# Performance work log

Hardware: AMD Instinct MI355X
Metric: run time of the kernel (lower is better)

Reference implementation:

```python
import jax, jax.numpy as jnp
import numpy as np

B, S, D = 2, 11253, 256
NHEAD, NLEVEL, DFF = 8, 4, 1024
KERNEL = 2
NPOINT = KERNEL * KERNEL
HEAD_DIM = D // NHEAD
LEVEL_SHAPES = [(92, 92), (46, 46), (23, 23), (12, 12)]
LEVEL_STARTS = np.cumsum([0] + [h * w for h, w in LEVEL_SHAPES])[:-1]


def _kernel_indices():
    # BoxeR _create_kernel_indices: even kernel -> [-0.5, 0.5]/K, (x, y) order
    idx = np.arange(KERNEL, dtype=np.float32) - (KERNEL - 1) / 2.0
    i, j = np.meshgrid(idx, idx, indexing="ij")
    return jnp.asarray(np.stack([j, i], -1).reshape(-1, 2) / KERNEL)


KIDX = _kernel_indices()  # (NPOINT, 2) box-relative sample offsets


def layer_norm(x, w, b, eps=1e-5):
    mu = x.mean(-1, keepdims=True)
    var = ((x - mu) ** 2).mean(-1, keepdims=True)
    return (x - mu) * jax.lax.rsqrt(var + eps) * w + b


def setup_inputs() -> dict:
    key = jax.random.key(0)
    ks = jax.random.split(key, 12)

    def p(i, shape, scale=0.02):
        return jax.random.normal(ks[i], shape, jnp.float32) * scale

    cxcy = jax.random.uniform(ks[2], (B, S, 2), jnp.float32, minval=0.1, maxval=0.9)
    wh = jax.random.uniform(ks[3], (B, S, 2), jnp.float32, minval=0.02, maxval=0.2)
    return dict(
        src=jax.random.normal(ks[0], (B, S, D), jnp.float32),
        pos=jax.random.normal(ks[1], (B, S, D), jnp.float32),
        src_shape=jnp.asarray(np.array(LEVEL_SHAPES, np.int32)),
        src_mask=jnp.zeros((B, S), jnp.bool_),
        src_start_index=jnp.asarray(LEVEL_STARTS.astype(np.int32)),
        src_valid_ratios=jnp.ones((B, NLEVEL, 2), jnp.float32),
        ref_windows=jnp.concatenate([cxcy, wh], -1),
        value_w=p(4, (D, D)), value_b=jnp.zeros((D,), jnp.float32),
        out_w=p(5, (D, D)), out_b=jnp.zeros((D,), jnp.float32),
        box_w=p(6, (NHEAD * NLEVEL * 4, D)), box_b=jnp.zeros((NHEAD * NLEVEL * 4,), jnp.float32),
        attn_w=p(7, (NHEAD * NLEVEL * NPOINT, D)), attn_b=jnp.zeros((NHEAD * NLEVEL * NPOINT,), jnp.float32),
        lin1_w=p(8, (DFF, D)), lin1_b=jnp.zeros((DFF,), jnp.float32),
        lin2_w=p(9, (D, DFF)), lin2_b=jnp.zeros((D,), jnp.float32),
        norm1_w=jnp.ones((D,), jnp.float32), norm1_b=jnp.zeros((D,), jnp.float32),
        norm2_w=jnp.ones((D,), jnp.float32), norm2_b=jnp.zeros((D,), jnp.float32),
    )


def box_attention(q, src, src_mask, src_valid_ratios, ref_windows,
                  value_w, value_b, out_w, out_b, box_w, box_b, attn_w, attn_b):
    value = src @ value_w.T + value_b
    value = jnp.where(src_mask[..., None], 0.0, value)
    value = value.reshape(B, S, NHEAD, HEAD_DIM)

    # where-to-attend: per-head, per-level box offsets decoded around ref_windows (cx,cy,w,h)
    off = (q @ box_w.T + box_b).reshape(B, S, NHEAD, NLEVEL, 4)
    ref = ref_windows[:, :, None, None, :]
    boxes = ref + off / 8.0 * ref[..., jnp.array([2, 3, 2, 3])]
    center, size = boxes[..., None, :2], boxes[..., None, 2:]
    grid = center + KIDX * jax.nn.relu(size)  # (B,S,nh,L,P,2) in normalized [0,1] coords
    grid = grid * src_valid_ratios[:, None, None, :, None, :]

    attn = (q @ attn_w.T + attn_b).reshape(B, S, NHEAD, NLEVEL * NPOINT)
    attn = jax.nn.softmax(attn, -1).reshape(B, S, NHEAD, NLEVEL, NPOINT)

    out = jnp.zeros((B, NHEAD, S, HEAD_DIM), src.dtype)
    for lvl, (H, W) in enumerate(LEVEL_SHAPES):
        s0 = int(LEVEL_STARTS[lvl])
        v = jnp.transpose(value[:, s0:s0 + H * W], (0, 2, 1, 3))  # (B,nh,HW,hd)
        loc = jnp.transpose(grid[:, :, :, lvl], (0, 2, 1, 3, 4))  # (B,nh,S,P,2)
        # grid_sample bilinear, align_corners=False, zero padding
        px = loc[..., 0] * W - 0.5
        py = loc[..., 1] * H - 0.5
        x0, y0 = jnp.floor(px), jnp.floor(py)
        wx, wy = (px - x0)[..., None], (py - y0)[..., None]

        def gather(ix, iy):
            valid = (ix >= 0) & (ix < W) & (iy >= 0) & (iy < H)
            idx = (jnp.clip(iy, 0, H - 1) * W + jnp.clip(ix, 0, W - 1)).astype(jnp.int32)
            g = jnp.take_along_axis(v, idx.reshape(B, NHEAD, S * NPOINT)[..., None], axis=2)
            return g.reshape(B, NHEAD, S, NPOINT, HEAD_DIM) * valid[..., None]

        g00, g01 = gather(x0, y0), gather(x0 + 1, y0)
        g10, g11 = gather(x0, y0 + 1), gather(x0 + 1, y0 + 1)
        samp = (g00 * (1 - wx) + g01 * wx) * (1 - wy) + (g10 * (1 - wx) + g11 * wx) * wy
        aw = jnp.transpose(attn[:, :, :, lvl], (0, 2, 1, 3))  # (B,nh,S,P)
        out = out + jnp.einsum("bhspd,bhsp->bhsd", samp, aw)

    out = jnp.transpose(out, (0, 2, 1, 3)).reshape(B, S, D)
    return out @ out_w.T + out_b


def reference(src, pos, src_shape, src_mask, src_start_index, src_valid_ratios,
              ref_windows, value_w, value_b, out_w, out_b, box_w, box_b,
              attn_w, attn_b, lin1_w, lin1_b, lin2_w, lin2_b,
              norm1_w, norm1_b, norm2_w, norm2_b):
    # self-attn (box attention) + residual + LN
    src2 = box_attention(src + pos, src, src_mask, src_valid_ratios, ref_windows,
                         value_w, value_b, out_w, out_b, box_w, box_b, attn_w, attn_b)
    x = layer_norm(src + src2, norm1_w, norm1_b)
    # FFN + residual + LN (dropout=0 in eval)
    ff = jax.nn.relu(x @ lin1_w.T + lin1_b) @ lin2_w.T + lin2_b
    return layer_norm(x + ff, norm2_w, norm2_b)
```

## Files before the change

### kernel.cpp

```cpp
#include <hip/hip_runtime.h>
#include <hip/hip_bf16.h>
#include <hip/hip_fp16.h>

#define TOKENS 22506
#define SLEN   11253

typedef __bf16 bf16x8 __attribute__((ext_vector_type(8)));
typedef float  f32x4  __attribute__((ext_vector_type(4)));
typedef float  f32x2  __attribute__((ext_vector_type(2)));
typedef uint   u32x4  __attribute__((ext_vector_type(4)));

#if defined(__has_builtin)
#if __has_builtin(__builtin_amdgcn_cvt_pk_f32_fp8) && __has_builtin(__builtin_amdgcn_cvt_pk_fp8_f32)
#define HAS_FP8CVT 1
#endif
#endif

__device__ __forceinline__ ushort f2bu(float f) {
    __hip_bfloat16 h = __float2bfloat16(f);
    return *reinterpret_cast<ushort*>(&h);
}
__device__ __forceinline__ float bu2f(ushort u) {
    return __uint_as_float((uint)u << 16);
}
__device__ __forceinline__ uint pkf16(float a, float b) {
    __half2 h = __floats2half2_rn(a, b);
    return *reinterpret_cast<uint*>(&h);
}
__device__ __forceinline__ void gl16(const ushort* g, ushort* l) {
    __builtin_amdgcn_global_load_lds(
        (__attribute__((address_space(1))) void*)(g),
        (__attribute__((address_space(3))) void*)(l), 16, 0, 0);
}

#ifndef HAS_FP8CVT
__device__ __forceinline__ uint enc_fp8(float x) {
    if (!(fabsf(x) >= 0.f)) return 0;
    uint u = __float_as_uint(x);
    uint s = (u >> 24) & 0x80u;
    float ax = fabsf(x);
    if (ax >= 448.f) return s | 0x7Eu;
    if (ax < 0.0009765625f) return s;
    int e; frexpf(ax, &e);
    int ue = e - 1;
    if (ue < -6) {
        int m = (int)(ax * 512.f + 0.5f);
        if (m > 7) m = 7;
        return s | (uint)m;
    }
    float q = ax * exp2f((float)(3 - ue));
    int mi = (int)(q + 0.5f);
    if (mi >= 16) { mi >>= 1; ++ue; if (ue > 8) return s | 0x7Eu; }
    return s | ((uint)(ue + 7) << 3) | ((uint)mi & 7u);
}
__device__ __forceinline__ float dec_fp8(uint b) {
    const float sgn = (b & 0x80u) ? -1.f : 1.f;
    const uint e = (b >> 3) & 15u, m = b & 7u;
    if (e == 0) return sgn * (float)m * 0.001953125f;
    return sgn * (1.0f + (float)m * 0.125f) * exp2f((float)e - 7.f);
}
#endif

__device__ __forceinline__ uint fp8pack4(float f0, float f1, float f2, float f3) {
#ifdef HAS_FP8CVT
    int p = 0;
    p = __builtin_amdgcn_cvt_pk_fp8_f32(f0, f1, p, false);
    p = __builtin_amdgcn_cvt_pk_fp8_f32(f2, f3, p, true);
    return (uint)p;
#else
    return enc_fp8(f0) | (enc_fp8(f1) << 8) | (enc_fp8(f2) << 16) | (enc_fp8(f3) << 24);
#endif
}
template<bool HI>
__device__ __forceinline__ f32x2 fp8pair(uint w) {
#ifdef HAS_FP8CVT
    auto c = __builtin_amdgcn_cvt_pk_f32_fp8((int)w, HI);
    f32x2 r; r.x = c[0]; r.y = c[1]; return r;
#else
    const uint sh = HI ? 16u : 0u;
    f32x2 r; r.x = dec_fp8((w >> sh) & 0xFFu); r.y = dec_fp8((w >> (sh + 8)) & 0xFFu);
    return r;
#endif
}

template<bool RELU, bool NTSTORE, bool F8Z0>
__global__ __launch_bounds__(256) void gemm_small(
    const ushort* __restrict__ A0, const ushort* __restrict__ W0,
    const float* __restrict__ b0, void* __restrict__ C0,
    const ushort* __restrict__ A1, const ushort* __restrict__ W1,
    const float* __restrict__ b1, void* __restrict__ C1,
    int M, int N, int K)
{
    const bool zz = blockIdx.z != 0;
    const ushort* A   = zz ? A1 : A0;
    const ushort* W   = zz ? W1 : W0;
    const float* bias = zz ? b1 : b0;
    void* Cptr        = zz ? C1 : C0;

    __shared__ ushort smem[12288];
    const int tid  = threadIdx.x;
    const int lane = tid & 63;
    const int wid  = tid >> 6;
    const int wr = wid >> 1, wc = wid & 1;
    const int m0 = blockIdx.x * 64, n0 = blockIdx.y * 128;
    const int lrow = lane & 15, lhi = lane >> 4;

    const int arow = tid >> 2;
    const int scol = (tid & 3) << 3;
    const ushort* ga  = A + (size_t)min(m0 + arow, M - 1) * K + scol;
    const ushort* gb0 = W + (size_t)(n0 + arow)      * K + scol;
    const ushort* gb1 = W + (size_t)(n0 + arow + 64) * K + scol;

    f32x4 acc[2][4] = {};
    const int NT = K >> 5;

    gl16(ga,  &smem[tid * 8]);
    gl16(gb0, &smem[4096 + tid * 8]);
    gl16(gb1, &smem[4096 + tid * 8 + 2048]);

    int cur = 0;
    for (int t = 0; t < NT; ++t) {
        __syncthreads();
        if (t + 1 < NT) {
            const int k0 = (t + 1) << 5;
            const int nb = cur ^ 1;
            gl16(ga  + k0, &smem[nb * 2048 + tid * 8]);
            gl16(gb0 + k0, &smem[4096 + nb * 4096 + tid * 8]);
            gl16(gb1 + k0, &smem[4096 + nb * 4096 + tid * 8 + 2048]);
        }
        bf16x8 afr[2], bfr[4];
        #pragma unroll
        for (int m = 0; m < 2; ++m)
            afr[m] = *reinterpret_cast<const bf16x8*>(
                &smem[cur * 2048 + (wr * 32 + m * 16 + lrow) * 32 + lhi * 8]);
        #pragma unroll
        for (int n = 0; n < 4; ++n)
            bfr[n] = *reinterpret_cast<const bf16x8*>(
                &smem[4096 + cur * 4096 + (wc * 64 + n * 16 + lrow) * 32 + lhi * 8]);
        #pragma unroll
        for (int m = 0; m < 2; ++m)
            #pragma unroll
            for (int n = 0; n < 4; ++n)
                acc[m][n] = __builtin_amdgcn_mfma_f32_16x16x32_bf16(
                    afr[m], bfr[n], acc[m][n], 0, 0, 0);
        cur ^= 1;
    }

    __syncthreads();
    #pragma unroll
    for (int m = 0; m < 2; ++m) {
        #pragma unroll
        for (int n = 0; n < 4; ++n) {
            const int col = wc * 64 + n * 16 + lrow;
            const float bv = bias[n0 + col];
            #pragma unroll
            for (int r = 0; r < 4; ++r) {
                const int row = wr * 32 + m * 16 + lhi * 4 + r;
                float v = acc[m][n][r] + bv;
                if (RELU) v = fmaxf(v, 0.f);
                smem[row * 136 + col] = f2bu(v);
            }
        }
    }
    __syncthreads();
    if (F8Z0 && !zz) {
        #pragma unroll
        for (int i = 0; i < 4; ++i) {
            const int e = tid + i * 256;
            const int row = e >> 4, ch = e & 15;
            if (m0 + row < M) {
                const u32x4 v = *reinterpret_cast<const u32x4*>(&smem[row * 136 + ch * 8]);
                float f[8];
                #pragma unroll
                for (int j = 0; j < 4; ++j) {
                    f[2 * j]     = __uint_as_float(v[j] << 16);
                    f[2 * j + 1] = __uint_as_float(v[j] & 0xFFFF0000u);
                }
                uint2 o;
                o.x = fp8pack4(f[0], f[1], f[2], f[3]);
                o.y = fp8pack4(f[4], f[5], f[6], f[7]);
                *reinterpret_cast<uint2*>(
                    (unsigned char*)Cptr + (size_t)(m0 + row) * N + n0 + ch * 8) = o;
            }
        }
    } else {
        #pragma unroll
        for (int i = 0; i < 4; ++i) {
            const int e = tid + i * 256;
            const int row = e >> 4, ch = e & 15;
            if (m0 + row < M) {
                const u32x4 v = *reinterpret_cast<const u32x4*>(&smem[row * 136 + ch * 8]);
                u32x4* dst = reinterpret_cast<u32x4*>(
                    (ushort*)Cptr + (size_t)(m0 + row) * N + n0 + ch * 8);
                if (NTSTORE) __builtin_nontemporal_store(v, dst);
                else *dst = v;
            }
        }
    }
}

__global__ __launch_bounds__(256) void prep_all(
    const float* __restrict__ vw, const float* __restrict__ bw,
    const float* __restrict__ aw, const float* __restrict__ ow,
    const float* __restrict__ l1, const float* __restrict__ l2,
    const float* __restrict__ bb, const float* __restrict__ ab,
    ushort* __restrict__ dstW, float* __restrict__ dstQB,
    const float4* __restrict__ src, const float4* __restrict__ pos,
    ushort4* __restrict__ srcb, ushort4* __restrict__ qb)
{
    const int blk = blockIdx.x;
    if (blk < 2817) {
        const int i = blk * 256 + threadIdx.x;
        if (i < 720896) {
            float v;
            if      (i <  65536) v = vw[i];
            else if (i <  98304) v = bw[i -  65536];
            else if (i < 131072) v = aw[i -  98304];
            else if (i < 196608) v = ow[i - 131072];
            else if (i < 458752) v = l1[i - 196608];
            else                 v = l2[i - 458752];
            dstW[i] = f2bu(v);
        } else if (i < 721152) {
            const int j = i - 720896;
            dstQB[j] = (j < 128) ? bb[j] : ab[j - 128];
        }
    } else {
        const int i = (blk - 2817) * 256 + threadIdx.x;
        if (i >= TOKENS * 64) return;
        const float4 s = src[i], p = pos[i];
        ushort4 us, uq;
        us.x = f2bu(s.x); us.y = f2bu(s.y); us.z = f2bu(s.z); us.w = f2bu(s.w);
        uq.x = f2bu(s.x + p.x); uq.y = f2bu(s.y + p.y);
        uq.z = f2bu(s.z + p.z); uq.w = f2bu(s.w + p.w);
        srcb[i] = us; qb[i] = uq;
    }
}

__global__ __launch_bounds__(256) void box_fused(
    const unsigned char* __restrict__ val,
    const ushort* __restrict__ qout,
    const float* __restrict__ refw,
    const float* __restrict__ vratio,
    ushort* __restrict__ attnout)
{
    __shared__ ushort4 offs[64 * 17];
    __shared__ uint2 wts[64 * 17];
    const int tid = threadIdx.x;

    int work;
    {
        const int x = blockIdx.x & 7, s = blockIdx.x >> 3;
        work = (x < 4) ? (s * 4 + x) : (1408 + s * 4 + (x - 4));
        if ((int)gridDim.x != 2814 || work >= (int)gridDim.x) work = blockIdx.x;
    }
    const int t0 = work * 8;

    {
        const int u = tid >> 2, lvl = tid & 3;
        const int t = min(t0 + (u >> 3), TOKENS - 1);
        const int h = u & 7;
        const int b = (t >= SLEN) ? 1 : 0;
        const ushort* qr = qout + (size_t)t * 256;

        const uint2 lu = *reinterpret_cast<const uint2*>(qr + 128 + h * 16 + lvl * 4);
        float e0 = __uint_as_float(lu.x << 16);
        float e1 = __uint_as_float(lu.x & 0xFFFF0000u);
        float e2 = __uint_as_float(lu.y << 16);
        float e3 = __uint_as_float(lu.y & 0xFFFF0000u);
        float mx = fmaxf(fmaxf(e0, e1), fmaxf(e2, e3));
        mx = fmaxf(mx, __shfl_xor(mx, 1));
        mx = fmaxf(mx, __shfl_xor(mx, 2));
        e0 = __expf(e0 - mx); e1 = __expf(e1 - mx);
        e2 = __expf(e2 - mx); e3 = __expf(e3 - mx);
        float ss = e0 + e1 + e2 + e3;
        ss += __shfl_xor(ss, 1);
        ss += __shfl_xor(ss, 2);
        const float inv = 1.f / ss;
        const float pe[4] = { e0 * inv, e1 * inv, e2 * inv, e3 * inv };

        const uint2 ou = *reinterpret_cast<const uint2*>(qr + h * 16 + lvl * 4);
        const float o0 = __uint_as_float(ou.x << 16) * 0.125f;
        const float o1 = __uint_as_float(ou.x & 0xFFFF0000u) * 0.125f;
        const float o2 = __uint_as_float(ou.y << 16) * 0.125f;
        const float o3 = __uint_as_float(ou.y & 0xFFFF0000u) * 0.125f;

        const float4 rw = *reinterpret_cast<const float4*>(refw + (size_t)t * 4);
        const int Ww = (lvl == 0) ? 92 : (lvl == 1) ? 46 : (lvl == 2) ? 23 : 12;
        const int s0 = (lvl == 0) ? 0 : (lvl == 1) ? 8464 : (lvl == 2) ? 10580 : 11109;
        const float vrx = vratio[(b * 4 + lvl) * 2 + 0];
        const float vry = vratio[(b * 4 + lvl) * 2 + 1];

        const float bx  = rw.x + o0 * rw.z;
        const float by  = rw.y + o1 * rw.w;
        const float bwd = fmaxf(rw.z + o2 * rw.z, 0.f);
        const float bhd = fmaxf(rw.w + o3 * rw.w, 0.f);

        #pragma unroll
        for (int k = 0; k < 4; ++k) {
            const float jx = (k & 1) ? 0.25f : -0.25f;
            const float iy = (k & 2) ? 0.25f : -0.25f;
            const float px = (bx + jx * bwd) * vrx * (float)Ww - 0.5f;
            const float py = (by + iy * bhd) * vry * (float)Ww - 0.5f;
            const float x0f = floorf(px), y0f = floorf(py);
            const int x0 = (int)x0f, y0 = (int)y0f;
            const float wx = px - x0f, wy = py - y0f;
            const float wp = pe[k];

            const bool vx0 = (x0 >= 0) && (x0 < Ww);
            const bool vx1 = (x0 + 1 >= 0) && (x0 + 1 < Ww);
            const bool vy0 = (y0 >= 0) && (y0 < Ww);
            const bool vy1 = (y0 + 1 >= 0) && (y0 + 1 < Ww);
            const int cx0 = min(max(x0, 0), Ww - 1);
            const int cx1 = min(max(x0 + 1, 0), Ww - 1);
            const int cy0 = min(max(y0, 0), Ww - 1);
            const int cy1 = min(max(y0 + 1, 0), Ww - 1);

            const float w00 = (vx0 && vy0) ? wp * (1.f - wx) * (1.f - wy) : 0.f;
            const float w01 = (vx1 && vy0) ? wp * wx         * (1.f - wy) : 0.f;
            const float w10 = (vx0 && vy1) ? wp * (1.f - wx) * wy         : 0.f;
            const float w11 = (vx1 && vy1) ? wp * wx         * wy         : 0.f;

            ushort4 sp;
            sp.x = (ushort)(s0 + cy0 * Ww + cx0);
            sp.y = (ushort)(s0 + cy0 * Ww + cx1);
            sp.z = (ushort)(s0 + cy1 * Ww + cx0);
            sp.w = (ushort)(s0 + cy1 * Ww + cx1);

            const int p = lvl * 4 + k;
            offs[u * 17 + p] = sp;
            wts[u * 17 + p]  = make_uint2(pkf16(w00, w01), pkf16(w10, w11));
        }
    }
    __syncthreads();

    const int u = tid >> 2, dl = tid & 3;
    const int traw = t0 + (u >> 3);
    const int t = min(traw, TOKENS - 1);
    const int h = u & 7;
    const uint boff = ((t >= SLEN) ? (uint)SLEN * 256u : 0u) + (uint)h * 32u + (uint)dl * 8u;
    const char* base = (const char*)val;

    const ushort4* po = &offs[u * 17];
    const uint2* pw = &wts[u * 17];
    f32x2 a0 = {0.f, 0.f}, a1 = {0.f, 0.f}, a2 = {0.f, 0.f}, a3 = {0.f, 0.f};

    #pragma unroll
    for (int g = 0; g < 8; ++g) {
        const ushort4 sA = po[g * 2 + 0];
        const ushort4 sB = po[g * 2 + 1];
        const uint2 wA = pw[g * 2 + 0];
        const uint2 wB = pw[g * 2 + 1];

        const uint2 v0 = *reinterpret_cast<const uint2*>(base + (((uint)sA.x << 8) + boff));
        const uint2 v1 = *reinterpret_cast<const uint2*>(base + (((uint)sA.y << 8) + boff));
        const uint2 v2 = *reinterpret_cast<const uint2*>(base + (((uint)sA.z << 8) + boff));
        const uint2 v3 = *reinterpret_cast<const uint2*>(base + (((uint)sA.w << 8) + boff));
        const uint2 v4 = *reinterpret_cast<const uint2*>(base + (((uint)sB.x << 8) + boff));
        const uint2 v5 = *reinterpret_cast<const uint2*>(base + (((uint)sB.y << 8) + boff));
        const uint2 v6 = *reinterpret_cast<const uint2*>(base + (((uint)sB.z << 8) + boff));
        const uint2 v7 = *reinterpret_cast<const uint2*>(base + (((uint)sB.w << 8) + boff));

        const float2 wAl = __half22float2(*reinterpret_cast<const __half2*>(&wA.x));
        const float2 wAh = __half22float2(*reinterpret_cast<const __half2*>(&wA.y));
        const float2 wBl = __half22float2(*reinterpret_cast<const __half2*>(&wB.x));
        const float2 wBh = __half22float2(*reinterpret_cast<const __half2*>(&wB.y));

        auto accf8 = [&](const uint2 v, const float w) {
            f32x2 wv; wv.x = w; wv.y = w;
            a0 += wv * fp8pair<false>(v.x);
            a1 += wv * fp8pair<true>(v.x);
            a2 += wv * fp8pair<false>(v.y);
            a3 += wv * fp8pair<true>(v.y);
        };
        accf8(v0, wAl.x); accf8(v1, wAl.y); accf8(v2, wAh.x); accf8(v3, wAh.y);
        accf8(v4, wBl.x); accf8(v5, wBl.y); accf8(v6, wBh.x); accf8(v7, wBh.y);
    }

    if (traw < TOKENS) {
        u32x4 o;
        o[0] = (uint)f2bu(a0.x) | ((uint)f2bu(a0.y) << 16);
        o[1] = (uint)f2bu(a1.x) | ((uint)f2bu(a1.y) << 16);
        o[2] = (uint)f2bu(a2.x) | ((uint)f2bu(a2.y) << 16);
        o[3] = (uint)f2bu(a3.x) | ((uint)f2bu(a3.y) << 16);
        *reinterpret_cast<u32x4*>(attnout + (size_t)t * 256 + h * 32 + dl * 8) = o;
    }
}

template<bool AF32, bool OUTF32>
__global__ __launch_bounds__(256) void ln_add2(
    const void* __restrict__ aptr, const ushort* __restrict__ bptr,
    const float* __restrict__ w, const float* __restrict__ bias,
    void* __restrict__ outp, int nrows)
{
    const int lane = threadIdx.x & 63, wv = threadIdx.x >> 6;
    const int row = blockIdx.x * 4 + wv;
    if (row >= nrows) return;
    const size_t base = (size_t)row * 256 + lane * 4;

    float4 av;
    if (AF32) {
        av = *reinterpret_cast<const float4*>((const float*)aptr + base);
    } else {
        const ushort4 u = *reinterpret_cast<const ushort4*>((const ushort*)aptr + base);
        av = make_float4(bu2f(u.x), bu2f(u.y), bu2f(u.z), bu2f(u.w));
    }
    const ushort4 ub = *reinterpret_cast<const ushort4*>(bptr + base);
    const float v0 = av.x + bu2f(ub.x), v1 = av.y + bu2f(ub.y);
    const float v2 = av.z + bu2f(ub.z), v3 = av.w + bu2f(ub.w);

    float s = v0 + v1 + v2 + v3;
    #pragma unroll
    for (int o = 32; o; o >>= 1) s += __shfl_xor(s, o);
    const float mu = s * (1.f / 256.f);
    const float d0 = v0 - mu, d1 = v1 - mu, d2 = v2 - mu, d3 = v3 - mu;
    float s2 = d0 * d0 + d1 * d1 + d2 * d2 + d3 * d3;
    #pragma unroll
    for (int o = 32; o; o >>= 1) s2 += __shfl_xor(s2, o);
    const float rs = rsqrtf(s2 * (1.f / 256.f) + 1e-5f);

    const float4 w4 = *reinterpret_cast<const float4*>(w + lane * 4);
    const float4 g4 = *reinterpret_cast<const float4*>(bias + lane * 4);
    const float r0 = d0 * rs * w4.x + g4.x;
    const float r1 = d1 * rs * w4.y + g4.y;
    const float r2 = d2 * rs * w4.z + g4.z;
    const float r3 = d3 * rs * w4.w + g4.w;
    if (OUTF32) {
        *reinterpret_cast<float4*>((float*)outp + base) = make_float4(r0, r1, r2, r3);
    } else {
        ushort4 u;
        u.x = f2bu(r0); u.y = f2bu(r1); u.z = f2bu(r2); u.w = f2bu(r3);
        *reinterpret_cast<ushort4*>((ushort*)outp + base) = u;
    }
}

extern "C" void kernel_launch(void* const* d_in, const int* in_sizes, int n_in,
                              void* d_out, int out_size, void* d_ws, size_t ws_size,
                              hipStream_t stream)
{
    const float* src     = (const float*)d_in[0];
    const float* pos     = (const float*)d_in[1];
    const float* vratio  = (const float*)d_in[5];
    const float* refw    = (const float*)d_in[6];
    const float* value_w = (const float*)d_in[7];
    const float* value_b = (const float*)d_in[8];
    const float* out_w   = (const float*)d_in[9];
    const float* out_b   = (const float*)d_in[10];
    const float* box_w   = (const float*)d_in[11];
    const float* box_b   = (const float*)d_in[12];
    const float* attn_w  = (const float*)d_in[13];
    const float* attn_b  = (const float*)d_in[14];
    const float* lin1_w  = (const float*)d_in[15];
    const float* lin1_b  = (const float*)d_in[16];
    const float* lin2_w  = (const float*)d_in[17];
    const float* lin2_b  = (const float*)d_in[18];
    const float* n1w     = (const float*)d_in[19];
    const float* n1b     = (const float*)d_in[20];
    const float* n2w     = (const float*)d_in[21];
    const float* n2b     = (const float*)d_in[22];

    char* wsb = (char*)d_ws;
    ushort* Wb    = (ushort*)(wsb);
    float*  qcb   = (float*)(wsb + 1441792);
    ushort* srcb  = (ushort*)(wsb + 1442816);
    ushort* qb    = (ushort*)(wsb + 12965888);
    unsigned char* valb = (unsigned char*)(wsb + 24488960);
    ushort* qoutb = (ushort*)(wsb + 36012032);
    ushort* attb  = (ushort*)(wsb + 47535104);
    ushort* src2b = (ushort*)(wsb + 59058176);
    ushort* xbb   = (ushort*)(wsb + 70581248);
    ushort* hb    = (ushort*)(wsb + 82104320);
    ushort* yb    = (ushort*)(wsb + 128196608);

    const dim3 blk(256);

    prep_all<<<dim3(8444), blk, 0, stream>>>(
        value_w, box_w, attn_w, out_w, lin1_w, lin2_w, box_b, attn_b, Wb, qcb,
        (const float4*)src, (const float4*)pos, (ushort4*)srcb, (ushort4*)qb);

    gemm_small<false, false, true><<<dim3(352, 2, 2), blk, 0, stream>>>(
        srcb, Wb, value_b, valb,
        qb, Wb + 65536, qcb, qoutb, TOKENS, 256, 256);

    box_fused<<<dim3((TOKENS + 7) / 8), blk, 0, stream>>>(
        valb, qoutb, refw, vratio, attb);

    gemm_small<false, false, false><<<dim3(352, 2, 1), blk, 0, stream>>>(
        attb, Wb + 131072, out_b, src2b,
        attb, Wb + 131072, out_b, src2b, TOKENS, 256, 256);
    ln_add2<false, false><<<dim3((TOKENS + 3) / 4), blk, 0, stream>>>(
        srcb, src2b, n1w, n1b, xbb, TOKENS);
    gemm_small<true, true, false><<<dim3(352, 8, 1), blk, 0, stream>>>(
        xbb, Wb + 196608, lin1_b, hb,
        xbb, Wb + 196608, lin1_b, hb, TOKENS, 1024, 256);
    gemm_small<false, false, false><<<dim3(352, 2, 1), blk, 0, stream>>>(
        hb, Wb + 458752, lin2_b, yb,
        hb, Wb + 458752, lin2_b, yb, TOKENS, 256, 1024);
    ln_add2<false, true><<<dim3((TOKENS + 3) / 4), blk, 0, stream>>>(
        xbb, yb, n2w, n2b, (float*)d_out, TOKENS);
}
```

Baseline: 133.6 us.

## Store FFN hidden activations in fp8 and run second FFN GEMM with fp8 MFMA

The first FFN GEMM now writes its ReLU output as fp8 instead of bf16, using non-temporal stores. The lin2 weights are converted to fp8 during prep. A new gemm_f8 kernel runs the second FFN GEMM with fp8 MFMA instructions and double-buffered LDS loads. This halves the bytes of the large hidden tensor that are written and read back, and doubles MFMA throughput on that GEMM, at the cost of lower precision in the FFN output.

New measurement: 131.3 us. About the same (-1.7%).

```diff
diff --git a/kernel.cpp b/kernel.cpp
--- a/kernel.cpp
+++ b/kernel.cpp
@@ -9,6 +9,7 @@
 typedef float  f32x4  __attribute__((ext_vector_type(4)));
 typedef float  f32x2  __attribute__((ext_vector_type(2)));
 typedef uint   u32x4  __attribute__((ext_vector_type(4)));
+typedef uint   u32x2  __attribute__((ext_vector_type(2)));
 
 #if defined(__has_builtin)
 #if __has_builtin(__builtin_amdgcn_cvt_pk_f32_fp8) && __has_builtin(__builtin_amdgcn_cvt_pk_fp8_f32)
@@ -27,7 +28,7 @@
     __half2 h = __floats2half2_rn(a, b);
     return *reinterpret_cast<uint*>(&h);
 }
-__device__ __forceinline__ void gl16(const ushort* g, ushort* l) {
+__device__ __forceinline__ void gl16(const void* g, void* l) {
     __builtin_amdgcn_global_load_lds(
         (__attribute__((address_space(1))) void*)(g),
         (__attribute__((address_space(3))) void*)(l), 16, 0, 0);
@@ -71,6 +72,13 @@
     return enc_fp8(f0) | (enc_fp8(f1) << 8) | (enc_fp8(f2) << 16) | (enc_fp8(f3) << 24);
 #endif
 }
+__device__ __forceinline__ uint fp8pack1(float f) {
+#ifdef HAS_FP8CVT
+    return (uint)__builtin_amdgcn_cvt_pk_fp8_f32(f, f, 0, false) & 0xFFu;
+#else
+    return enc_fp8(f);
+#endif
+}
 template<bool HI>
 __device__ __forceinline__ f32x2 fp8pair(uint w) {
 #ifdef HAS_FP8CVT
@@ -176,11 +184,13 @@
                     f[2 * j]     = __uint_as_float(v[j] << 16);
                     f[2 * j + 1] = __uint_as_float(v[j] & 0xFFFF0000u);
                 }
-                uint2 o;
-                o.x = fp8pack4(f[0], f[1], f[2], f[3]);
-                o.y = fp8pack4(f[4], f[5], f[6], f[7]);
-                *reinterpret_cast<uint2*>(
-                    (unsigned char*)Cptr + (size_t)(m0 + row) * N + n0 + ch * 8) = o;
+                u32x2 o;
+                o[0] = fp8pack4(f[0], f[1], f[2], f[3]);
+                o[1] = fp8pack4(f[4], f[5], f[6], f[7]);
+                u32x2* dst = reinterpret_cast<u32x2*>(
+                    (unsigned char*)Cptr + (size_t)(m0 + row) * N + n0 + ch * 8);
+                if (NTSTORE) __builtin_nontemporal_store(o, dst);
+                else *dst = o;
             }
         }
     } else {
@@ -199,12 +209,91 @@
     }
 }
 
+__global__ __launch_bounds__(256) void gemm_f8(
+    const unsigned char* __restrict__ A, const unsigned char* __restrict__ W,
+    const float* __restrict__ bias, ushort* __restrict__ C,
+    int M, int N, int K)
+{
+    __shared__ unsigned char smem[17408];
+    const int tid  = threadIdx.x;
+    const int lane = tid & 63;
+    const int wid  = tid >> 6;
+    const int wr = wid >> 1, wc = wid & 1;
+    const int m0 = blockIdx.x * 64, n0 = blockIdx.y * 128;
+    const int lrow = lane & 15, lhi = lane >> 4;
+
+    const int arow = tid >> 1;
+    const int achk = (tid & 1) << 4;
+    const unsigned char* ga = A + (size_t)min(m0 + (arow & 63), M - 1) * K + achk;
+    const unsigned char* gb = W + (size_t)(n0 + arow) * K + achk;
+
+    f32x4 acc[2][4] = {};
+    const int NT = K >> 5;
+
+    if (tid < 128) gl16(ga, &smem[tid * 16]);
+    gl16(gb, &smem[4096 + tid * 16]);
+
+    int cur = 0;
+    for (int t = 0; t < NT; ++t) {
+        __syncthreads();
+        if (t + 1 < NT) {
+            const int k0 = (t + 1) << 5;
+            const int nb = cur ^ 1;
+            if (tid < 128) gl16(ga + k0, &smem[nb * 2048 + tid * 16]);
+            gl16(gb + k0, &smem[4096 + nb * 4096 + tid * 16]);
+        }
+        long afr[2], bfr[4];
+        #pragma unroll
+        for (int m = 0; m < 2; ++m)
+            afr[m] = *reinterpret_cast<const long*>(
+                &smem[cur * 2048 + (wr * 32 + m * 16 + lrow) * 32 + lhi * 8]);
+        #pragma unroll
+        for (int n = 0; n < 4; ++n)
+            bfr[n] = *reinterpret_cast<const long*>(
+                &smem[4096 + cur * 4096 + (wc * 64 + n * 16 + lrow) * 32 + lhi * 8]);
+        #pragma unroll
+        for (int m = 0; m < 2; ++m)
+            #pragma unroll
+            for (int n = 0; n < 4; ++n)
+                acc[m][n] = __builtin_amdgcn_mfma_f32_16x16x32_fp8_fp8(
+                    afr[m], bfr[n], acc[m][n], 0, 0, 0);
+        cur ^= 1;
+    }
+
+    __syncthreads();
+    ushort* sm16 = reinterpret_cast<ushort*>(smem);
+    #pragma unroll
+    for (int m = 0; m < 2; ++m) {
+        #pragma unroll
+        for (int n = 0; n < 4; ++n) {
+            const int col = wc * 64 + n * 16 + lrow;
+            const float bv = bias[n0 + col];
+            #pragma unroll
+            for (int r = 0; r < 4; ++r) {
+                const int row = wr * 32 + m * 16 + lhi * 4 + r;
+                sm16[row * 136 + col] = f2bu(acc[m][n][r] + bv);
+            }
+        }
+    }
+    __syncthreads();
+    #pragma unroll
+    for (int i = 0; i < 4; ++i) {
+        const int e = tid + i * 256;
+        const int row = e >> 4, ch = e & 15;
+        if (m0 + row < M) {
+            const u32x4 v = *reinterpret_cast<const u32x4*>(&sm16[row * 136 + ch * 8]);
+            *reinterpret_cast<u32x4*>(C + (size_t)(m0 + row) * N + n0 + ch * 8) = v;
+        }
+    }
+}
+
 __global__ __launch_bounds__(256) void prep_all(
     const float* __restrict__ vw, const float* __restrict__ bw,
     const float* __restrict__ aw, const float* __restrict__ ow,
     const float* __restrict__ l1, const float* __restrict__ l2,
     const float* __restrict__ bb, const float* __restrict__ ab,
     ushort* __restrict__ dstW, float* __restrict__ dstQB,
+    unsigned char* __restrict__ dstW8,
     const float4* __restrict__ src, const float4* __restrict__ pos,
     ushort4* __restrict__ srcb, ushort4* __restrict__ qb)
 {
@@ -220,6 +309,7 @@
             else if (i < 458752) v = l1[i - 196608];
             else                 v = l2[i - 458752];
             dstW[i] = f2bu(v);
+            if (i >= 458752) dstW8[i - 458752] = (unsigned char)fp8pack1(v);
         } else if (i < 721152) {
             const int j = i - 720896;
             dstQB[j] = (j < 128) ? bb[j] : ab[j - 128];
@@ -468,14 +558,15 @@
     ushort* attb  = (ushort*)(wsb + 47535104);
     ushort* src2b = (ushort*)(wsb + 59058176);
     ushort* xbb   = (ushort*)(wsb + 70581248);
-    ushort* hb    = (ushort*)(wsb + 82104320);
-    ushort* yb    = (ushort*)(wsb + 128196608);
+    unsigned char* hb8 = (unsigned char*)(wsb + 82104320);
+    ushort* yb    = (ushort*)(wsb + 105150464);
+    unsigned char* Wf8 = (unsigned char*)(wsb + 116673536);
 
     const dim3 blk(256);
 
     prep_all<<<dim3(8444), blk, 0, stream>>>(
         value_w, box_w, attn_w, out_w, lin1_w, lin2_w, box_b, attn_b, Wb, qcb,
-        (const float4*)src, (const float4*)pos, (ushort4*)srcb, (ushort4*)qb);
+        Wf8, (const float4*)src, (const float4*)pos, (ushort4*)srcb, (ushort4*)qb);
 
     gemm_small<false, false, true><<<dim3(352, 2, 2), blk, 0, stream>>>(
         srcb, Wb, value_b, valb,
@@ -489,12 +580,11 @@
         attb, Wb + 131072, out_b, src2b, TOKENS, 256, 256);
     ln_add2<false, false><<<dim3((TOKENS + 3) / 4), blk, 0, stream>>>(
         srcb, src2b, n1w, n1b, xbb, TOKENS);
-    gemm_small<true, true, false><<<dim3(352, 8, 1), blk, 0, stream>>>(
-        xbb, Wb + 196608, lin1_b, hb,
-        xbb, Wb + 196608, lin1_b, hb, TOKENS, 1024, 256);
-    gemm_small<false, false, false><<<dim3(352, 2, 1), blk, 0, stream>>>(
-        hb, Wb + 458752, lin2_b, yb,
-        hb, Wb + 458752, lin2_b, yb, TOKENS, 256, 1024);
+    gemm_small<true, true, true><<<dim3(352, 8, 1), blk, 0, stream>>>(
+        xbb, Wb + 196608, lin1_b, hb8,
+        xbb, Wb + 196608, lin1_b, hb8, TOKENS, 1024, 256);
+    gemm_f8<<<dim3(352, 2), blk, 0, stream>>>(
+        hb8, Wf8, lin2_b, yb, TOKENS, 256, 1024);
     ln_add2<false, true><<<dim3((TOKENS + 3) / 4), blk, 0, stream>>>(
         xbb, yb, n2w, n2b, (float*)d_out, TOKENS);
 }
```
